# Optimization experiments

Hardware: AMD Instinct MI355X
Metric: run time of the kernel (lower is better)

The kernel has to match this reference:

```python
import jax, jax.numpy as jnp
import numpy as np

N = 100000
E = 1600000
F_IN, F_HID, F_OUT = 128, 128, 128


def setup_inputs() -> dict:
    key = jax.random.key(0)
    k = jax.random.split(key, 6)
    x = jax.random.normal(k[0], (N, F_IN), dtype=jnp.float32)
    edge_index = jax.random.randint(k[1], (2, E), 0, N, dtype=jnp.int32)
    # Glorot-style scaled weights (values arbitrary for a correctness baseline)
    W1 = jax.random.normal(k[2], (F_IN, F_HID), dtype=jnp.float32) * (1.0 / np.sqrt(F_IN))
    b1 = jnp.zeros((F_HID,), dtype=jnp.float32)
    W2 = jax.random.normal(k[3], (F_HID, F_OUT), dtype=jnp.float32) * (1.0 / np.sqrt(F_HID))
    b2 = jnp.zeros((F_OUT,), dtype=jnp.float32)
    return {"x": x, "edge_index": edge_index, "W1": W1, "b1": b1, "W2": W2, "b2": b2}


def _gcn_conv(x, src, dst, norm, W, b, num_nodes):
    # PyG GCNConv: h = x @ W; out_i = sum_j norm_ij * h_j ; out += b
    h = x @ W                                   # [N, F_out]
    msgs = h[src] * norm[:, None]               # [E', F_out] gather + scale
    agg = jax.ops.segment_sum(msgs, dst, num_segments=num_nodes)  # scatter-add
    return agg + b


def reference(x, edge_index, W1, b1, W2, b2):
    num_nodes = x.shape[0]
    # add self-loops (GCNConv default add_self_loops=True)
    loops = jnp.arange(num_nodes, dtype=edge_index.dtype)
    src = jnp.concatenate([edge_index[0], loops])
    dst = jnp.concatenate([edge_index[1], loops])
    # symmetric normalization: deg computed with self-loops, edge weight 1
    deg = jax.ops.segment_sum(jnp.ones_like(src, dtype=x.dtype), dst, num_segments=num_nodes)
    dinv = jnp.where(deg > 0, jax.lax.rsqrt(deg), 0.0)
    norm = dinv[src] * dinv[dst]                # [E']

    h = jax.nn.relu(_gcn_conv(x, src, dst, norm, W1, b1, num_nodes))
    out = _gcn_conv(h, src, dst, norm, W2, b2, num_nodes)
    return out
```

## Files before the change

### kernel.cpp

```cpp
#include <hip/hip_runtime.h>


typedef __attribute__((ext_vector_type(8))) short bf16x8;
typedef __attribute__((ext_vector_type(4))) float f32x4;
typedef unsigned int uint;
typedef unsigned short ushort;

#define BKT_SHIFT 9
#define BKT_NODES 512
#define TPE 16

__device__ __forceinline__ ushort f2bf(float f) {
  union { float f; uint u; } c; c.f = f;
  uint u = c.u;
  uint r = u + 0x7fffu + ((u >> 16) & 1u);
  return (ushort)(r >> 16);
}
__device__ __forceinline__ float bf_lo(uint u) {
  union { uint i; float f; } c; c.i = u << 16; return c.f;
}
__device__ __forceinline__ float bf_hi(uint u) {
  union { uint i; float f; } c; c.i = u & 0xffff0000u; return c.f;
}


__global__ __launch_bounds__(256) void k_bktscatter(const int* __restrict__ src,
                                                    const int* __restrict__ dst,
                                                    int* __restrict__ bcur,
                                                    uint* __restrict__ ebuf,
                                                    int E, int nbk, int cap) {
  __shared__ int h[1024];
  __shared__ int rbase[1024];
  int t = threadIdx.x;
  for (int i = t; i < nbk; i += 256) h[i] = 0;
  __syncthreads();
  int beg = blockIdx.x * (256 * TPE);
  int d[TPE], s[TPE];
#pragma unroll
  for (int j = 0; j < TPE; ++j) {
    int e = beg + j * 256 + t;
    bool v = e < E;
    d[j] = v ? dst[e] : -1;
    s[j] = v ? src[e] : 0;
    if (v) atomicAdd(&h[d[j] >> BKT_SHIFT], 1);
  }
  __syncthreads();
  for (int i = t; i < nbk; i += 256) {
    int c = h[i];
    rbase[i] = c ? atomicAdd(&bcur[i], c) : 0;
    h[i] = 0;
  }
  __syncthreads();
#pragma unroll
  for (int j = 0; j < TPE; ++j) {
    if (d[j] >= 0) {
      int b = d[j] >> BKT_SHIFT;
      int rel = rbase[b] + atomicAdd(&h[b], 1);
      if (rel < cap)
        ebuf[(size_t)b * cap + rel] =
            ((uint)s[j] << BKT_SHIFT) | (uint)(d[j] & (BKT_NODES - 1));
    }
  }
}

__global__ __launch_bounds__(1024) void k_bktscan(const int* __restrict__ bcur,
                                                  int* __restrict__ bbase,
                                                  int nbk, int cap,
                                                  int* __restrict__ row_ptr, int N) {
  __shared__ int s[1024];
  int t = threadIdx.x;
  int c = 0;
  if (t < nbk) c = min(bcur[t], cap);
  s[t] = c;
  __syncthreads();
  for (int off = 1; off < 1024; off <<= 1) {
    int u = 0;
    if (t >= off) u = s[t - off];
    __syncthreads();
    if (t >= off) s[t] += u;
    __syncthreads();
  }
  if (t < nbk) bbase[t] = s[t] - c;
  if (t == nbk - 1) { bbase[nbk] = s[t]; row_ptr[N] = s[t]; }
}

__global__ __launch_bounds__(256) void k_bktcsr(const uint* __restrict__ ebuf,
                                                const int* __restrict__ bbase,
                                                int cap,
                                                int* __restrict__ row_ptr,
                                                float* __restrict__ dinv,
                                                int* __restrict__ csr_src, int N) {
  __shared__ int ncnt[BKT_NODES];
  __shared__ int nscan[BKT_NODES];
  __shared__ int ncur[BKT_NODES];
  __shared__ int wtot[4];
  int t = threadIdx.x;
  int b = blockIdx.x;
  int node0 = b << BKT_SHIFT;
  int ebase = bbase[b];
  int cnt = bbase[b + 1] - ebase;
  const uint* ein = ebuf + (size_t)b * cap;
  ncnt[t] = 0; ncnt[t + 256] = 0;
  ncur[t] = 0; ncur[t + 256] = 0;
  __syncthreads();
  for (int e = t; e < cnt; e += 256)
    atomicAdd(&ncnt[ein[e] & (BKT_NODES - 1)], 1);
  __syncthreads();
  int v0 = ncnt[2 * t], v1 = ncnt[2 * t + 1];
  int s = v0 + v1;
  int lane = t & 63, wv = t >> 6;
  int inc = s;
#pragma unroll
  for (int off = 1; off < 64; off <<= 1) {
    int u = __shfl_up(inc, off);
    if (lane >= off) inc += u;
  }
  if (lane == 63) wtot[wv] = inc;
  __syncthreads();
  int woff = 0;
  for (int i = 0; i < wv; ++i) woff += wtot[i];
  int ex = woff + inc - s;
  nscan[2 * t] = ex;
  nscan[2 * t + 1] = ex + v0;
  int n0 = node0 + 2 * t;
  if (n0 < N) {
    row_ptr[n0] = ebase + ex;
    dinv[n0] = rsqrtf((float)v0 + 1.0f);
  }
  if (n0 + 1 < N) {
    row_ptr[n0 + 1] = ebase + ex + v0;
    dinv[n0 + 1] = rsqrtf((float)v1 + 1.0f);
  }
  __syncthreads();
  for (int e = t; e < cnt; e += 256) {
    uint u = ein[e];
    int l = u & (BKT_NODES - 1);
    int pos = ebase + nscan[l] + atomicAdd(&ncur[l], 1);
    csr_src[pos] = (int)(u >> BKT_SHIFT);
  }
}


__device__ __forceinline__ bf16x8 pack8(float4 u, float4 v) {
  bf16x8 r;
  r[0] = (short)f2bf(u.x); r[1] = (short)f2bf(u.y);
  r[2] = (short)f2bf(u.z); r[3] = (short)f2bf(u.w);
  r[4] = (short)f2bf(v.x); r[5] = (short)f2bf(v.y);
  r[6] = (short)f2bf(v.z); r[7] = (short)f2bf(v.w);
  return r;
}

template <bool A_IS_F32>
__global__ __launch_bounds__(256) void k_gemm_mfma(const void* __restrict__ A,
                                                   const float* __restrict__ Wf,
                                                   const float* __restrict__ dinv,
                                                   ushort* __restrict__ H, int n) {
  __shared__ __align__(16) ushort Bt[16 * 128 * 8];
  int t = threadIdx.x;
  for (int id = t; id < 16 * 128; id += 256) {
    int col = id & 127, ch = id >> 7;
    ushort us[8];
#pragma unroll
    for (int j = 0; j < 8; ++j) us[j] = f2bf(Wf[(ch * 8 + j) * 128 + col]);
    uint4 p;
    p.x = (uint)us[0] | ((uint)us[1] << 16);
    p.y = (uint)us[2] | ((uint)us[3] << 16);
    p.z = (uint)us[4] | ((uint)us[5] << 16);
    p.w = (uint)us[6] | ((uint)us[7] << 16);
    *(uint4*)&Bt[id * 8] = p;
  }
  __syncthreads();

  int wv = t >> 6, lane = t & 63;
  int r16 = lane & 15, kg = lane >> 4;
  int row0 = blockIdx.x * 128 + wv * 32;
  f32x4 acc[2][8] = {};

#pragma unroll
  for (int ks = 0; ks < 4; ++ks) {
    bf16x8 a0, a1;
    if (A_IS_F32) {
      const float* Af = (const float*)A;
      int r = min(row0 + r16, n - 1);
      const float* p = &Af[(size_t)r * 128 + ks * 32 + kg * 8];
      a0 = pack8(*(const float4*)p, *(const float4*)(p + 4));
      r = min(row0 + 16 + r16, n - 1);
      p = &Af[(size_t)r * 128 + ks * 32 + kg * 8];
      a1 = pack8(*(const float4*)p, *(const float4*)(p + 4));
    } else {
      const ushort* Ab = (const ushort*)A;
      int r = min(row0 + r16, n - 1);
      a0 = *(const bf16x8*)&Ab[(size_t)r * 128 + ks * 32 + kg * 8];
      r = min(row0 + 16 + r16, n - 1);
      a1 = *(const bf16x8*)&Ab[(size_t)r * 128 + ks * 32 + kg * 8];
    }
#pragma unroll
    for (int tc = 0; tc < 8; ++tc) {
      bf16x8 b = *(const bf16x8*)&Bt[(((ks * 4 + kg) * 128) + tc * 16 + r16) * 8];
      acc[0][tc] = __builtin_amdgcn_mfma_f32_16x16x32_bf16(a0, b, acc[0][tc], 0, 0, 0);
      acc[1][tc] = __builtin_amdgcn_mfma_f32_16x16x32_bf16(a1, b, acc[1][tc], 0, 0, 0);
    }
  }

#pragma unroll
  for (int rt = 0; rt < 2; ++rt)
#pragma unroll
    for (int rg = 0; rg < 4; ++rg) {
      int row = row0 + rt * 16 + kg * 4 + rg;
      if (row < n) {
        float dv = dinv[row];
#pragma unroll
        for (int tc = 0; tc < 8; ++tc)
          H[(size_t)row * 128 + tc * 16 + r16] = f2bf(dv * acc[rt][tc][rg]);
      }
    }
}


__device__ __forceinline__ void add8(uint4 u, float* a) {
  a[0] += bf_lo(u.x); a[1] += bf_hi(u.x);
  a[2] += bf_lo(u.y); a[3] += bf_hi(u.y);
  a[4] += bf_lo(u.z); a[5] += bf_hi(u.z);
  a[6] += bf_lo(u.w); a[7] += bf_hi(u.w);
}

template <int MODE>
__global__ __launch_bounds__(256) void k_aggregate(
    const ushort* __restrict__ H, const int* __restrict__ csr_src,
    const int* __restrict__ row_ptr, const float* __restrict__ dinv,
    const float* __restrict__ bias, ushort* __restrict__ outb,
    float* __restrict__ outf, int n) {
  int wave = (blockIdx.x * blockDim.x + threadIdx.x) >> 6;
  int lane = threadIdx.x & 63;
  int sub = lane >> 4, c16 = lane & 15;
  int node = wave * 4 + sub;
  bool valid = node < n;
  int nd = valid ? node : (n - 1);

  float di = dinv[nd];
  int beg = row_ptr[nd];
  int end = valid ? row_ptr[nd + 1] : beg;

  float acc[8] = {};
  uint4 sv = *(const uint4*)&H[(size_t)nd * 128 + c16 * 8];
  add8(sv, acc);

  int e = beg;
  for (; e + 7 < end; e += 8) {
    int s[8];
    uint4 u[8];
#pragma unroll
    for (int j = 0; j < 8; ++j) s[j] = csr_src[e + j];
#pragma unroll
    for (int j = 0; j < 8; ++j)
      u[j] = *(const uint4*)&H[(size_t)s[j] * 128 + c16 * 8];
#pragma unroll
    for (int j = 0; j < 8; ++j) add8(u[j], acc);
  }
  for (; e + 3 < end; e += 4) {
    int s0 = csr_src[e], s1 = csr_src[e + 1];
    int s2 = csr_src[e + 2], s3 = csr_src[e + 3];
    uint4 u0 = *(const uint4*)&H[(size_t)s0 * 128 + c16 * 8];
    uint4 u1 = *(const uint4*)&H[(size_t)s1 * 128 + c16 * 8];
    uint4 u2 = *(const uint4*)&H[(size_t)s2 * 128 + c16 * 8];
    uint4 u3 = *(const uint4*)&H[(size_t)s3 * 128 + c16 * 8];
    add8(u0, acc); add8(u1, acc); add8(u2, acc); add8(u3, acc);
  }
  for (; e < end; ++e) {
    int s0 = csr_src[e];
    uint4 u0 = *(const uint4*)&H[(size_t)s0 * 128 + c16 * 8];
    add8(u0, acc);
  }

  float4 bA = *(const float4*)&bias[c16 * 8];
  float4 bB = *(const float4*)&bias[c16 * 8 + 4];
  float o[8];
  o[0] = fmaf(di, acc[0], bA.x); o[1] = fmaf(di, acc[1], bA.y);
  o[2] = fmaf(di, acc[2], bA.z); o[3] = fmaf(di, acc[3], bA.w);
  o[4] = fmaf(di, acc[4], bB.x); o[5] = fmaf(di, acc[5], bB.y);
  o[6] = fmaf(di, acc[6], bB.z); o[7] = fmaf(di, acc[7], bB.w);

  if (!valid) return;
  if (MODE == 0) {
#pragma unroll
    for (int i = 0; i < 8; ++i) o[i] = fmaxf(o[i], 0.f);
    uint4 w;
    w.x = (uint)f2bf(o[0]) | ((uint)f2bf(o[1]) << 16);
    w.y = (uint)f2bf(o[2]) | ((uint)f2bf(o[3]) << 16);
    w.z = (uint)f2bf(o[4]) | ((uint)f2bf(o[5]) << 16);
    w.w = (uint)f2bf(o[6]) | ((uint)f2bf(o[7]) << 16);
    *(uint4*)&outb[(size_t)node * 128 + c16 * 8] = w;
  } else {
    *(float4*)&outf[(size_t)node * 128 + c16 * 8] =
        make_float4(o[0], o[1], o[2], o[3]);
    *(float4*)&outf[(size_t)node * 128 + c16 * 8 + 4] =
        make_float4(o[4], o[5], o[6], o[7]);
  }
}


extern "C" void kernel_launch(void* const* d_in, const int* in_sizes, int n_in,
                              void* d_out, int out_size, void* d_ws, size_t ws_size,
                              hipStream_t stream) {
  const float* x  = (const float*)d_in[0];
  const int* eidx = (const int*)d_in[1];
  const float* W1 = (const float*)d_in[2];
  const float* b1 = (const float*)d_in[3];
  const float* W2 = (const float*)d_in[4];
  const float* b2 = (const float*)d_in[5];
  float* out = (float*)d_out;

  const int N = in_sizes[0] / 128;
  const int E = in_sizes[1] / 2;
  const int* src = eidx;
  const int* dst = eidx + E;
  const int NBK = (N + BKT_NODES - 1) >> BKT_SHIFT;
  const int CAP = (((E / NBK) * 3 / 2) + 255) & ~255;

  auto align16 = [](size_t v) { return (v + 15) & ~(size_t)15; };
  char* w = (char*)d_ws;
  ushort* hb    = (ushort*)w; w += align16((size_t)N * 128 * 2);
  ushort* h1b   = (ushort*)w; w += align16((size_t)N * 128 * 2);
  int* csr_src  = (int*)w;    w += align16((size_t)E * 4);
  int* row_ptr  = (int*)w;    w += align16((size_t)(N + 1) * 4);
  float* dinv   = (float*)w;  w += align16((size_t)N * 4);
  int* bbase    = (int*)w;    w += align16((size_t)(NBK + 1) * 4);
  int* bcur     = (int*)w;    w += align16((size_t)(NBK + 1) * 4);
  uint* ebuf = (uint*)h1b;

  hipMemsetAsync(bcur, 0, (size_t)NBK * 4, stream);
  const int SCB = (E + 256 * TPE - 1) / (256 * TPE);
  k_bktscatter<<<SCB, 256, 0, stream>>>(src, dst, bcur, ebuf, E, NBK, CAP);
  k_bktscan<<<1, 1024, 0, stream>>>(bcur, bbase, NBK, CAP, row_ptr, N);
  k_bktcsr<<<NBK, 256, 0, stream>>>(ebuf, bbase, CAP, row_ptr, dinv, csr_src, N);

  const int GB = (N + 127) / 128;
  const int AGG_BLOCKS = ((N + 3) / 4 + 3) / 4;
  k_gemm_mfma<true><<<GB, 256, 0, stream>>>(x, W1, dinv, hb, N);
  k_aggregate<0><<<AGG_BLOCKS, 256, 0, stream>>>(
      hb, csr_src, row_ptr, dinv, b1, h1b, nullptr, N);
  k_gemm_mfma<false><<<GB, 256, 0, stream>>>(h1b, W2, dinv, hb, N);
  k_aggregate<1><<<AGG_BLOCKS, 256, 0, stream>>>(
      hb, csr_src, row_ptr, dinv, b2, nullptr, out, N);
}
```

Before: 221.0 us.

## Sort nodes by degree within buckets to balance aggregation waves

Inside each 512-node bucket, the CSR build kernel now computes a counting sort of nodes by in-degree and writes a permutation array. Both aggregation kernels process nodes in that order, so the four nodes sharing a wave have similar degrees and spend less time diverged. Outputs are written to the permuted node index, which makes the stores less sequential. The edges-per-thread constant of the bucket scatter is also doubled, halving its grid.

```diff
diff --git a/kernel.cpp b/kernel.cpp
--- a/kernel.cpp
+++ b/kernel.cpp
@@ -8,7 +8,7 @@
 
 #define BKT_SHIFT 9
 #define BKT_NODES 512
-#define TPE 16
+#define TPE 32
 
 __device__ __forceinline__ ushort f2bf(float f) {
   union { float f; uint u; } c; c.f = f;
@@ -89,10 +89,14 @@
                                                 int cap,
                                                 int* __restrict__ row_ptr,
                                                 float* __restrict__ dinv,
-                                                int* __restrict__ csr_src, int N) {
+                                                int* __restrict__ csr_src,
+                                                int* __restrict__ order, int N) {
   __shared__ int ncnt[BKT_NODES];
   __shared__ int nscan[BKT_NODES];
   __shared__ int ncur[BKT_NODES];
+  __shared__ int dhist[BKT_NODES];
+  __shared__ int dbase[BKT_NODES];
+  __shared__ int dcur[BKT_NODES];
   __shared__ int wtot[4];
   int t = threadIdx.x;
   int b = blockIdx.x;
@@ -102,6 +106,8 @@
   const uint* ein = ebuf + (size_t)b * cap;
   ncnt[t] = 0; ncnt[t + 256] = 0;
   ncur[t] = 0; ncur[t + 256] = 0;
+  dhist[t] = 0; dhist[t + 256] = 0;
+  dcur[t] = 0; dcur[t + 256] = 0;
   __syncthreads();
   for (int e = t; e < cnt; e += 256)
     atomicAdd(&ncnt[ein[e] & (BKT_NODES - 1)], 1);
@@ -131,12 +137,40 @@
     row_ptr[n0 + 1] = ebase + ex + v0;
     dinv[n0 + 1] = rsqrtf((float)v1 + 1.0f);
   }
+  int d0 = min(v0, BKT_NODES - 1), d1 = min(v1, BKT_NODES - 1);
+  if (n0 < N) atomicAdd(&dhist[d0], 1);
+  if (n0 + 1 < N) atomicAdd(&dhist[d1], 1);
   __syncthreads();
   for (int e = t; e < cnt; e += 256) {
     uint u = ein[e];
     int l = u & (BKT_NODES - 1);
     int pos = ebase + nscan[l] + atomicAdd(&ncur[l], 1);
     csr_src[pos] = (int)(u >> BKT_SHIFT);
+  }
+  int w0 = dhist[2 * t], w1 = dhist[2 * t + 1];
+  int ss = w0 + w1;
+  int inc2 = ss;
+#pragma unroll
+  for (int off = 1; off < 64; off <<= 1) {
+    int u = __shfl_up(inc2, off);
+    if (lane >= off) inc2 += u;
+  }
+  __syncthreads();
+  if (lane == 63) wtot[wv] = inc2;
+  __syncthreads();
+  int woff2 = 0;
+  for (int i = 0; i < wv; ++i) woff2 += wtot[i];
+  int ex2 = woff2 + inc2 - ss;
+  dbase[2 * t] = ex2;
+  dbase[2 * t + 1] = ex2 + w0;
+  __syncthreads();
+  if (n0 < N) {
+    int p = dbase[d0] + atomicAdd(&dcur[d0], 1);
+    order[node0 + p] = n0;
+  }
+  if (n0 + 1 < N) {
+    int p = dbase[d1] + atomicAdd(&dcur[d1], 1);
+    order[node0 + p] = n0 + 1;
   }
 }
 
@@ -228,14 +262,15 @@
 __global__ __launch_bounds__(256) void k_aggregate(
     const ushort* __restrict__ H, const int* __restrict__ csr_src,
     const int* __restrict__ row_ptr, const float* __restrict__ dinv,
+    const int* __restrict__ order,
     const float* __restrict__ bias, ushort* __restrict__ outb,
     float* __restrict__ outf, int n) {
   int wave = (blockIdx.x * blockDim.x + threadIdx.x) >> 6;
   int lane = threadIdx.x & 63;
   int sub = lane >> 4, c16 = lane & 15;
-  int node = wave * 4 + sub;
-  bool valid = node < n;
-  int nd = valid ? node : (n - 1);
+  int idx = wave * 4 + sub;
+  bool valid = idx < n;
+  int nd = valid ? order[idx] : (n - 1);
 
   float di = dinv[nd];
   int beg = row_ptr[nd];
@@ -289,11 +324,11 @@
     w.y = (uint)f2bf(o[2]) | ((uint)f2bf(o[3]) << 16);
     w.z = (uint)f2bf(o[4]) | ((uint)f2bf(o[5]) << 16);
     w.w = (uint)f2bf(o[6]) | ((uint)f2bf(o[7]) << 16);
-    *(uint4*)&outb[(size_t)node * 128 + c16 * 8] = w;
+    *(uint4*)&outb[(size_t)nd * 128 + c16 * 8] = w;
   } else {
-    *(float4*)&outf[(size_t)node * 128 + c16 * 8] =
+    *(float4*)&outf[(size_t)nd * 128 + c16 * 8] =
         make_float4(o[0], o[1], o[2], o[3]);
-    *(float4*)&outf[(size_t)node * 128 + c16 * 8 + 4] =
+    *(float4*)&outf[(size_t)nd * 128 + c16 * 8 + 4] =
         make_float4(o[4], o[5], o[6], o[7]);
   }
 }
@@ -324,6 +359,7 @@
   int* csr_src  = (int*)w;    w += align16((size_t)E * 4);
   int* row_ptr  = (int*)w;    w += align16((size_t)(N + 1) * 4);
   float* dinv   = (float*)w;  w += align16((size_t)N * 4);
+  int* order    = (int*)w;    w += align16((size_t)N * 4);
   int* bbase    = (int*)w;    w += align16((size_t)(NBK + 1) * 4);
   int* bcur     = (int*)w;    w += align16((size_t)(NBK + 1) * 4);
   uint* ebuf = (uint*)h1b;
@@ -332,14 +368,15 @@
   const int SCB = (E + 256 * TPE - 1) / (256 * TPE);
   k_bktscatter<<<SCB, 256, 0, stream>>>(src, dst, bcur, ebuf, E, NBK, CAP);
   k_bktscan<<<1, 1024, 0, stream>>>(bcur, bbase, NBK, CAP, row_ptr, N);
-  k_bktcsr<<<NBK, 256, 0, stream>>>(ebuf, bbase, CAP, row_ptr, dinv, csr_src, N);
+  k_bktcsr<<<NBK, 256, 0, stream>>>(ebuf, bbase, CAP, row_ptr, dinv, csr_src,
+                                    order, N);
 
   const int GB = (N + 127) / 128;
   const int AGG_BLOCKS = ((N + 3) / 4 + 3) / 4;
   k_gemm_mfma<true><<<GB, 256, 0, stream>>>(x, W1, dinv, hb, N);
   k_aggregate<0><<<AGG_BLOCKS, 256, 0, stream>>>(
-      hb, csr_src, row_ptr, dinv, b1, h1b, nullptr, N);
+      hb, csr_src, row_ptr, dinv, order, b1, h1b, nullptr, N);
   k_gemm_mfma<false><<<GB, 256, 0, stream>>>(h1b, W2, dinv, hb, N);
   k_aggregate<1><<<AGG_BLOCKS, 256, 0, stream>>>(
-      hb, csr_src, row_ptr, dinv, b2, nullptr, out, N);
-}
+      hb, csr_src, row_ptr, dinv, order, b2, nullptr, out, N);
+}
```

After: 236.8 us. 7.2% more time.

## Drop bucket scan kernel using padded per-bucket CSR with (start,count) row info

Applied to the files above, without the earlier changes.

Removes the single-block prefix-scan kernel by laying out CSR edges in fixed-capacity per-bucket slots, so each row is described by an int2 (start, count) instead of a compact row_ptr. The aggregation kernels read this int2 and use nontemporal loads for edge indices and nontemporal stores for outputs. Edges per scatter thread are doubled (TPE 16 to 32), which halves the scatter grid. The aim is to cut one launch and serialization point and to reduce cache pollution, at the cost of a larger sparse csr_src buffer and 8-byte row metadata.

```diff
diff --git a/kernel.cpp b/kernel.cpp
--- a/kernel.cpp
+++ b/kernel.cpp
@@ -3,12 +3,13 @@
 
 typedef __attribute__((ext_vector_type(8))) short bf16x8;
 typedef __attribute__((ext_vector_type(4))) float f32x4;
+typedef __attribute__((ext_vector_type(4))) unsigned int u32x4;
 typedef unsigned int uint;
 typedef unsigned short ushort;
 
 #define BKT_SHIFT 9
 #define BKT_NODES 512
-#define TPE 16
+#define TPE 32
 
 __device__ __forceinline__ ushort f2bf(float f) {
   union { float f; uint u; } c; c.f = f;
@@ -63,31 +64,10 @@
   }
 }
 
-__global__ __launch_bounds__(1024) void k_bktscan(const int* __restrict__ bcur,
-                                                  int* __restrict__ bbase,
-                                                  int nbk, int cap,
-                                                  int* __restrict__ row_ptr, int N) {
-  __shared__ int s[1024];
-  int t = threadIdx.x;
-  int c = 0;
-  if (t < nbk) c = min(bcur[t], cap);
-  s[t] = c;
-  __syncthreads();
-  for (int off = 1; off < 1024; off <<= 1) {
-    int u = 0;
-    if (t >= off) u = s[t - off];
-    __syncthreads();
-    if (t >= off) s[t] += u;
-    __syncthreads();
-  }
-  if (t < nbk) bbase[t] = s[t] - c;
-  if (t == nbk - 1) { bbase[nbk] = s[t]; row_ptr[N] = s[t]; }
-}
-
 __global__ __launch_bounds__(256) void k_bktcsr(const uint* __restrict__ ebuf,
-                                                const int* __restrict__ bbase,
+                                                const int* __restrict__ bcur,
                                                 int cap,
-                                                int* __restrict__ row_ptr,
+                                                int2* __restrict__ rowinfo,
                                                 float* __restrict__ dinv,
                                                 int* __restrict__ csr_src, int N) {
   __shared__ int ncnt[BKT_NODES];
@@ -97,9 +77,9 @@
   int t = threadIdx.x;
   int b = blockIdx.x;
   int node0 = b << BKT_SHIFT;
-  int ebase = bbase[b];
-  int cnt = bbase[b + 1] - ebase;
-  const uint* ein = ebuf + (size_t)b * cap;
+  int ebase = b * cap;
+  int cnt = min(bcur[b], cap);
+  const uint* ein = ebuf + (size_t)ebase;
   ncnt[t] = 0; ncnt[t + 256] = 0;
   ncur[t] = 0; ncur[t + 256] = 0;
   __syncthreads();
@@ -124,11 +104,11 @@
   nscan[2 * t + 1] = ex + v0;
   int n0 = node0 + 2 * t;
   if (n0 < N) {
-    row_ptr[n0] = ebase + ex;
+    rowinfo[n0] = make_int2(ebase + ex, v0);
     dinv[n0] = rsqrtf((float)v0 + 1.0f);
   }
   if (n0 + 1 < N) {
-    row_ptr[n0 + 1] = ebase + ex + v0;
+    rowinfo[n0 + 1] = make_int2(ebase + ex + v0, v1);
     dinv[n0 + 1] = rsqrtf((float)v1 + 1.0f);
   }
   __syncthreads();
@@ -227,7 +207,7 @@
 template <int MODE>
 __global__ __launch_bounds__(256) void k_aggregate(
     const ushort* __restrict__ H, const int* __restrict__ csr_src,
-    const int* __restrict__ row_ptr, const float* __restrict__ dinv,
+    const int2* __restrict__ rowinfo, const float* __restrict__ dinv,
     const float* __restrict__ bias, ushort* __restrict__ outb,
     float* __restrict__ outf, int n) {
   int wave = (blockIdx.x * blockDim.x + threadIdx.x) >> 6;
@@ -238,8 +218,9 @@
   int nd = valid ? node : (n - 1);
 
   float di = dinv[nd];
-  int beg = row_ptr[nd];
-  int end = valid ? row_ptr[nd + 1] : beg;
+  int2 ri = rowinfo[nd];
+  int beg = ri.x;
+  int end = beg + (valid ? ri.y : 0);
 
   float acc[8] = {};
   uint4 sv = *(const uint4*)&H[(size_t)nd * 128 + c16 * 8];
@@ -250,7 +231,7 @@
     int s[8];
     uint4 u[8];
 #pragma unroll
-    for (int j = 0; j < 8; ++j) s[j] = csr_src[e + j];
+    for (int j = 0; j < 8; ++j) s[j] = __builtin_nontemporal_load(&csr_src[e + j]);
 #pragma unroll
     for (int j = 0; j < 8; ++j)
       u[j] = *(const uint4*)&H[(size_t)s[j] * 128 + c16 * 8];
@@ -258,8 +239,10 @@
     for (int j = 0; j < 8; ++j) add8(u[j], acc);
   }
   for (; e + 3 < end; e += 4) {
-    int s0 = csr_src[e], s1 = csr_src[e + 1];
-    int s2 = csr_src[e + 2], s3 = csr_src[e + 3];
+    int s0 = __builtin_nontemporal_load(&csr_src[e]);
+    int s1 = __builtin_nontemporal_load(&csr_src[e + 1]);
+    int s2 = __builtin_nontemporal_load(&csr_src[e + 2]);
+    int s3 = __builtin_nontemporal_load(&csr_src[e + 3]);
     uint4 u0 = *(const uint4*)&H[(size_t)s0 * 128 + c16 * 8];
     uint4 u1 = *(const uint4*)&H[(size_t)s1 * 128 + c16 * 8];
     uint4 u2 = *(const uint4*)&H[(size_t)s2 * 128 + c16 * 8];
@@ -267,7 +250,7 @@
     add8(u0, acc); add8(u1, acc); add8(u2, acc); add8(u3, acc);
   }
   for (; e < end; ++e) {
-    int s0 = csr_src[e];
+    int s0 = __builtin_nontemporal_load(&csr_src[e]);
     uint4 u0 = *(const uint4*)&H[(size_t)s0 * 128 + c16 * 8];
     add8(u0, acc);
   }
@@ -284,17 +267,17 @@
   if (MODE == 0) {
 #pragma unroll
     for (int i = 0; i < 8; ++i) o[i] = fmaxf(o[i], 0.f);
-    uint4 w;
+    u32x4 w;
     w.x = (uint)f2bf(o[0]) | ((uint)f2bf(o[1]) << 16);
     w.y = (uint)f2bf(o[2]) | ((uint)f2bf(o[3]) << 16);
     w.z = (uint)f2bf(o[4]) | ((uint)f2bf(o[5]) << 16);
     w.w = (uint)f2bf(o[6]) | ((uint)f2bf(o[7]) << 16);
-    *(uint4*)&outb[(size_t)node * 128 + c16 * 8] = w;
+    __builtin_nontemporal_store(w, (u32x4*)&outb[(size_t)node * 128 + c16 * 8]);
   } else {
-    *(float4*)&outf[(size_t)node * 128 + c16 * 8] =
-        make_float4(o[0], o[1], o[2], o[3]);
-    *(float4*)&outf[(size_t)node * 128 + c16 * 8 + 4] =
-        make_float4(o[4], o[5], o[6], o[7]);
+    f32x4 oa = {o[0], o[1], o[2], o[3]};
+    f32x4 ob = {o[4], o[5], o[6], o[7]};
+    __builtin_nontemporal_store(oa, (f32x4*)&outf[(size_t)node * 128 + c16 * 8]);
+    __builtin_nontemporal_store(ob, (f32x4*)&outf[(size_t)node * 128 + c16 * 8 + 4]);
   }
 }
 
@@ -321,25 +304,23 @@
   char* w = (char*)d_ws;
   ushort* hb    = (ushort*)w; w += align16((size_t)N * 128 * 2);
   ushort* h1b   = (ushort*)w; w += align16((size_t)N * 128 * 2);
-  int* csr_src  = (int*)w;    w += align16((size_t)E * 4);
-  int* row_ptr  = (int*)w;    w += align16((size_t)(N + 1) * 4);
+  int* csr_src  = (int*)w;    w += align16((size_t)NBK * CAP * 4);
+  int2* rowinfo = (int2*)w;   w += align16((size_t)N * 8);
   float* dinv   = (float*)w;  w += align16((size_t)N * 4);
-  int* bbase    = (int*)w;    w += align16((size_t)(NBK + 1) * 4);
   int* bcur     = (int*)w;    w += align16((size_t)(NBK + 1) * 4);
   uint* ebuf = (uint*)h1b;
 
   hipMemsetAsync(bcur, 0, (size_t)NBK * 4, stream);
   const int SCB = (E + 256 * TPE - 1) / (256 * TPE);
   k_bktscatter<<<SCB, 256, 0, stream>>>(src, dst, bcur, ebuf, E, NBK, CAP);
-  k_bktscan<<<1, 1024, 0, stream>>>(bcur, bbase, NBK, CAP, row_ptr, N);
-  k_bktcsr<<<NBK, 256, 0, stream>>>(ebuf, bbase, CAP, row_ptr, dinv, csr_src, N);
+  k_bktcsr<<<NBK, 256, 0, stream>>>(ebuf, bcur, CAP, rowinfo, dinv, csr_src, N);
 
   const int GB = (N + 127) / 128;
   const int AGG_BLOCKS = ((N + 3) / 4 + 3) / 4;
   k_gemm_mfma<true><<<GB, 256, 0, stream>>>(x, W1, dinv, hb, N);
   k_aggregate<0><<<AGG_BLOCKS, 256, 0, stream>>>(
-      hb, csr_src, row_ptr, dinv, b1, h1b, nullptr, N);
+      hb, csr_src, rowinfo, dinv, b1, h1b, nullptr, N);
   k_gemm_mfma<false><<<GB, 256, 0, stream>>>(h1b, W2, dinv, hb, N);
   k_aggregate<1><<<AGG_BLOCKS, 256, 0, stream>>>(
-      hb, csr_src, row_ptr, dinv, b2, nullptr, out, N);
-}
+      hb, csr_src, rowinfo, dinv, b2, nullptr, out, N);
+}
```

After: 222.9 us. Within noise of the previous version (+0.9%).
